# Optimization experiments

Hardware: AMD Instinct MI355X
Metric: run time of the kernel (lower is better)

The kernel has to match this reference:

```python
import jax, jax.numpy as jnp
import numpy as np

N = 262144
D = 512
H = 512
G = 1024


def setup_inputs() -> dict:
    key = jax.random.key(0)
    k1, k2, k3, k4 = jax.random.split(key, 4)
    embed = jax.random.normal(k1, (N, D), dtype=jnp.float32)
    batch_index = jnp.sort(jax.random.randint(k2, (N,), 0, G)).astype(jnp.int64)
    # nn.Linear weights: W_att [atten_hidden, embed_size], V_att [1, atten_hidden]
    W_att = jax.random.normal(k3, (H, D), dtype=jnp.float32) * (1.0 / np.sqrt(D))
    V_att = jax.random.normal(k4, (1, H), dtype=jnp.float32) * (1.0 / np.sqrt(H))
    return {"embed": embed, "batch_index": batch_index, "W_att": W_att, "V_att": V_att, "num_segments": G}


def reference(embed, batch_index, W_att, V_att, num_segments):
    # beta = V(tanh(W(embed))).squeeze(-1)  -> [N]
    beta = jnp.einsum('nh,oh->no', jnp.tanh(jnp.einsum('nd,hd->nh', embed, W_att)), V_att).squeeze(-1)
    # segment softmax (unnormalized exp, as in the original module)
    exp_beta = jnp.exp(beta)
    grouped_sum = jax.ops.segment_sum(exp_beta, batch_index, num_segments=num_segments)  # [G]
    alpha = exp_beta / grouped_sum[batch_index]  # [N]
    # scatter-weighted sum of node embeddings per graph -> [G, D]
    result = jax.ops.segment_sum(alpha[:, None] * embed, batch_index, num_segments=num_segments)
    return result
```

## Files before the change

### kernel.cpp

```cpp
#include <hip/hip_runtime.h>
#include <hip/hip_bf16.h>

#define D_DIM 512
#define H_DIM 512
#define G_SEG 1024
#define BM    64

typedef __attribute__((ext_vector_type(8))) short bf16x8;
typedef __attribute__((ext_vector_type(4))) float f32x4;
typedef unsigned int u32;
typedef unsigned short u16;

#define WS_S   0
#define WS_WB  8192

#define AS_BYTES  (BM * 1024)
#define BETA_OFF  AS_BYTES
#define EBS_OFF   (BETA_OFF + 4 * BM * 4)
#define SIDX_OFF  (EBS_OFF + BM * 4)
#define SCR_OFF   (SIDX_OFF + BM * 4)
#define LDS_TOTAL (SCR_OFF + 4 * 512 * 4)

static __device__ __forceinline__ u16 f2bf(float f) {
    __hip_bfloat16 h = __float2bfloat16(f);
    return *(u16*)&h;
}
static __device__ __forceinline__ float bf2f(u16 u) {
    return __uint_as_float(((u32)u) << 16);
}
static __device__ __forceinline__ float fast_tanh(float x) {
    float e = exp2f(x * 2.885390081777927f);
    return 1.0f - 2.0f * __builtin_amdgcn_rcpf(e + 1.0f);
}
static __device__ __forceinline__ void pack8(const float4& a, const float4& b, void* dst) {
    u16 h[8];
    h[0]=f2bf(a.x); h[1]=f2bf(a.y); h[2]=f2bf(a.z); h[3]=f2bf(a.w);
    h[4]=f2bf(b.x); h[5]=f2bf(b.y); h[6]=f2bf(b.z); h[7]=f2bf(b.w);
    *(uint4*)dst = *(uint4*)h;
}

__global__ __launch_bounds__(256)
void cvt_w(const float* __restrict__ W, u16* __restrict__ Wb) {
    int t   = blockIdx.x * 256 + threadIdx.x;
    int lhi = t & 3;
    int c   = (t >> 2) & 511;
    int k32 = t >> 11;
    const float* src = W + (size_t)c * 512 + k32 * 32 + lhi * 8;
    float4 f0 = *(const float4*)(src);
    float4 f1 = *(const float4*)(src + 4);
    pack8(f0, f1, Wb + (size_t)t * 8);
}

__global__ __launch_bounds__(256, 2)
void fused(const float* __restrict__ E, const int* __restrict__ BI,
           const u16* __restrict__ Wb, const float* __restrict__ V,
           float* __restrict__ out, float* __restrict__ S)
{
    extern __shared__ char smem[];
    const int tid = threadIdx.x;
    const int nodeBase = blockIdx.x * BM;
    const int l   = tid & 63;
    const int w   = tid >> 6;
    const int l15 = l & 15;
    const int lhi = l >> 4;

    const float* Eb = E + (size_t)nodeBase * 512;

#pragma unroll 1
    for (int p = 0; p < 4; ++p) {
        float4 L[8];
        const int ci0 = p * 1024 + tid * 4;
#pragma unroll
        for (int j = 0; j < 4; ++j) {
            int ci = ci0 + j;
            int row = ci >> 6, cc = ci & 63;
            const float* src = Eb + (size_t)row * 512 + cc * 8;
            L[2*j]   = *(const float4*)src;
            L[2*j+1] = *(const float4*)(src + 4);
        }
#pragma unroll
        for (int j = 0; j < 4; ++j) {
            int ci = ci0 + j;
            int row = ci >> 6, cc = ci & 63;
            int byte0 = row * 1024 + ((cc * 16) ^ ((row & 7) << 4));
            pack8(L[2*j], L[2*j+1], smem + byte0);
        }
    }
    __syncthreads();

    f32x4 acc[4][8];
#pragma unroll
    for (int m = 0; m < 4; ++m)
#pragma unroll
        for (int n = 0; n < 8; ++n) acc[m][n] = (f32x4){0.f, 0.f, 0.f, 0.f};

    const int bOffBase = ((w * 128 + l15) * 4 + lhi) * 16;
    const char* Wbb = (const char*)Wb;

    bf16x8 bA[8], bB[8];
#pragma unroll
    for (int n = 0; n < 8; ++n)
        bA[n] = *(const bf16x8*)(Wbb + bOffBase + n * 1024);

#pragma unroll 1
    for (int kk2 = 0; kk2 < 8; ++kk2) {
        {
            const char* Wn = Wbb + ((size_t)(2 * kk2 + 1) << 15);
#pragma unroll
            for (int n = 0; n < 8; ++n)
                bB[n] = *(const bf16x8*)(Wn + bOffBase + n * 1024);
            bf16x8 a[4];
            const int kbyte = (2 * kk2) * 64 + lhi * 16;
#pragma unroll
            for (int m = 0; m < 4; ++m) {
                int row = m * 16 + l15;
                a[m] = *(const bf16x8*)(smem + row * 1024 + (kbyte ^ ((row & 7) << 4)));
            }
#pragma unroll
            for (int m = 0; m < 4; ++m)
#pragma unroll
                for (int n = 0; n < 8; ++n)
                    acc[m][n] = __builtin_amdgcn_mfma_f32_16x16x32_bf16(a[m], bA[n], acc[m][n], 0, 0, 0);
        }
        {
            if (kk2 < 7) {
                const char* Wn = Wbb + ((size_t)(2 * kk2 + 2) << 15);
#pragma unroll
                for (int n = 0; n < 8; ++n)
                    bA[n] = *(const bf16x8*)(Wn + bOffBase + n * 1024);
            }
            bf16x8 a[4];
            const int kbyte = (2 * kk2 + 1) * 64 + lhi * 16;
#pragma unroll
            for (int m = 0; m < 4; ++m) {
                int row = m * 16 + l15;
                a[m] = *(const bf16x8*)(smem + row * 1024 + (kbyte ^ ((row & 7) << 4)));
            }
#pragma unroll
            for (int m = 0; m < 4; ++m)
#pragma unroll
                for (int n = 0; n < 8; ++n)
                    acc[m][n] = __builtin_amdgcn_mfma_f32_16x16x32_bf16(a[m], bB[n], acc[m][n], 0, 0, 0);
        }
    }

    float Vv[8];
#pragma unroll
    for (int n = 0; n < 8; ++n)
        Vv[n] = V[w * 128 + n * 16 + l15];

    float bsum[4][4];
#pragma unroll
    for (int m = 0; m < 4; ++m)
#pragma unroll
        for (int r = 0; r < 4; ++r) {
            float s = 0.f;
#pragma unroll
            for (int n = 0; n < 8; ++n)
                s += Vv[n] * fast_tanh(acc[m][n][r]);
            bsum[m][r] = s;
        }
#pragma unroll
    for (int off = 1; off <= 8; off <<= 1)
#pragma unroll
        for (int m = 0; m < 4; ++m)
#pragma unroll
            for (int r = 0; r < 4; ++r)
                bsum[m][r] += __shfl_xor(bsum[m][r], off, 64);

    float* betaP = (float*)(smem + BETA_OFF);
    if (l15 == 0) {
#pragma unroll
        for (int m = 0; m < 4; ++m)
#pragma unroll
            for (int r = 0; r < 4; ++r)
                betaP[w * BM + m * 16 + lhi * 4 + r] = bsum[m][r];
    }
    __syncthreads();

    float* ebs  = (float*)(smem + EBS_OFF);
    int*   sidx = (int*)(smem + SIDX_OFF);
    if (tid < BM) {
        float beta = betaP[tid] + betaP[BM + tid] + betaP[2 * BM + tid] + betaP[3 * BM + tid];
        float eb = expf(beta);
        ebs[tid] = eb;
        int g = BI[nodeBase + tid];
        sidx[tid] = g;
        int g0 = __shfl(g, 0, 64);
        if (__all(g == g0)) {
            float s = eb;
#pragma unroll
            for (int off = 1; off <= 32; off <<= 1)
                s += __shfl_xor(s, off, 64);
            if (l == 0) atomicAdd(&S[g], s);
        } else {
            atomicAdd(&S[g], eb);
        }
    }
    __syncthreads();

    {
        float* scr = (float*)(smem + SCR_OFF) + w * 512;
        const int rbase = w * 16;
        float a8[8];
#pragma unroll
        for (int j = 0; j < 8; ++j) a8[j] = 0.f;
        int gcur = sidx[rbase];

#pragma unroll 1
        for (int rr = 0; rr < 16; ++rr) {
            int r = rbase + rr;
            int g = sidx[r];
            if (g != gcur) {
                *(float4*)(scr + l * 8)     = make_float4(a8[0], a8[1], a8[2], a8[3]);
                *(float4*)(scr + l * 8 + 4) = make_float4(a8[4], a8[5], a8[6], a8[7]);
                asm volatile("s_waitcnt lgkmcnt(0)" ::: "memory");
#pragma unroll
                for (int j = 0; j < 8; ++j)
                    atomicAdd(&out[(size_t)gcur * 512 + j * 64 + l], scr[j * 64 + l]);
#pragma unroll
                for (int j = 0; j < 8; ++j) a8[j] = 0.f;
                gcur = g;
            }
            float wgt = ebs[r];
            bf16x8 v = *(const bf16x8*)(smem + r * 1024 + ((l * 16) ^ ((r & 7) << 4)));
#pragma unroll
            for (int j = 0; j < 8; ++j)
                a8[j] += wgt * bf2f((u16)v[j]);
        }
        *(float4*)(scr + l * 8)     = make_float4(a8[0], a8[1], a8[2], a8[3]);
        *(float4*)(scr + l * 8 + 4) = make_float4(a8[4], a8[5], a8[6], a8[7]);
        asm volatile("s_waitcnt lgkmcnt(0)" ::: "memory");
#pragma unroll
        for (int j = 0; j < 8; ++j)
            atomicAdd(&out[(size_t)gcur * 512 + j * 64 + l], scr[j * 64 + l]);
    }
}

__global__ __launch_bounds__(256)
void finalize_kernel(float* __restrict__ out, const float* __restrict__ S) {
    int idx = blockIdx.x * 256 + threadIdx.x;
    float s = S[idx >> 9];
    float v = out[idx];
    out[idx] = (s != 0.f) ? v * __builtin_amdgcn_rcpf(s) : 0.f;
}

extern "C" void kernel_launch(void* const* d_in, const int* in_sizes, int n_in,
                              void* d_out, int out_size, void* d_ws, size_t ws_size,
                              hipStream_t stream) {
    const float* E  = (const float*)d_in[0];
    const int*   BI = (const int*)d_in[1];
    const float* W  = (const float*)d_in[2];
    const float* V  = (const float*)d_in[3];
    float* out = (float*)d_out;
    char*  ws  = (char*)d_ws;
    const int Ntot = in_sizes[0] / D_DIM;

    float* S  = (float*)(ws + WS_S);
    u16*   Wb = (u16*)(ws + WS_WB);

    hipMemsetAsync(S, 0, G_SEG * 4, stream);
    hipMemsetAsync(out, 0, (size_t)out_size * 4, stream);
    hipFuncSetAttribute((const void*)fused,
                        hipFuncAttributeMaxDynamicSharedMemorySize, LDS_TOTAL);

    cvt_w<<<128, 256, 0, stream>>>(W, Wb);
    fused<<<Ntot / BM, 256, LDS_TOTAL, stream>>>(E, BI, Wb, V, out, S);
    finalize_kernel<<<out_size / 256, 256, 0, stream>>>(out, S);
}
```

Before: 356.3 us.

## Split fused kernel into GEMM-beta pass and separate fp32 weighted-sum pass

```diff
diff --git a/kernel.cpp b/kernel.cpp
--- a/kernel.cpp
+++ b/kernel.cpp
@@ -11,22 +11,17 @@
 typedef unsigned int u32;
 typedef unsigned short u16;
 
-#define WS_S   0
-#define WS_WB  8192
+#define WS_S    0
+#define WS_BETA 8192
+#define WS_WB   (8192 + (1u << 20))
 
 #define AS_BYTES  (BM * 1024)
 #define BETA_OFF  AS_BYTES
-#define EBS_OFF   (BETA_OFF + 4 * BM * 4)
-#define SIDX_OFF  (EBS_OFF + BM * 4)
-#define SCR_OFF   (SIDX_OFF + BM * 4)
-#define LDS_TOTAL (SCR_OFF + 4 * 512 * 4)
+#define LDS_K1    (BETA_OFF + 4 * BM * 4)
 
 static __device__ __forceinline__ u16 f2bf(float f) {
     __hip_bfloat16 h = __float2bfloat16(f);
     return *(u16*)&h;
-}
-static __device__ __forceinline__ float bf2f(u16 u) {
-    return __uint_as_float(((u32)u) << 16);
 }
 static __device__ __forceinline__ float fast_tanh(float x) {
     float e = exp2f(x * 2.885390081777927f);
@@ -52,9 +47,8 @@
 }
 
 __global__ __launch_bounds__(256, 2)
-void fused(const float* __restrict__ E, const int* __restrict__ BI,
-           const u16* __restrict__ Wb, const float* __restrict__ V,
-           float* __restrict__ out, float* __restrict__ S)
+void gemm_beta(const float* __restrict__ E, const u16* __restrict__ Wb,
+               const float* __restrict__ V, float* __restrict__ betaOut)
 {
     extern __shared__ char smem[];
     const int tid = threadIdx.x;
@@ -178,63 +172,58 @@
     }
     __syncthreads();
 
-    float* ebs  = (float*)(smem + EBS_OFF);
-    int*   sidx = (int*)(smem + SIDX_OFF);
     if (tid < BM) {
         float beta = betaP[tid] + betaP[BM + tid] + betaP[2 * BM + tid] + betaP[3 * BM + tid];
-        float eb = expf(beta);
-        ebs[tid] = eb;
-        int g = BI[nodeBase + tid];
-        sidx[tid] = g;
+        betaOut[nodeBase + tid] = beta;
+    }
+}
+
+__global__ __launch_bounds__(256)
+void wsum_eb(const float* __restrict__ E, const int* __restrict__ BI,
+             const float* __restrict__ beta, float* __restrict__ S,
+             float* __restrict__ out)
+{
+    __shared__ float al[256];
+    __shared__ int   sg[256];
+    const int t = threadIdx.x;
+    const int base = blockIdx.x * 256;
+    {
+        int n = base + t;
+        float eb = expf(beta[n]);
+        al[t] = eb;
+        int g = BI[n];
+        sg[t] = g;
         int g0 = __shfl(g, 0, 64);
         if (__all(g == g0)) {
             float s = eb;
 #pragma unroll
             for (int off = 1; off <= 32; off <<= 1)
                 s += __shfl_xor(s, off, 64);
-            if (l == 0) atomicAdd(&S[g], s);
+            if ((t & 63) == 0) atomicAdd(&S[g], s);
         } else {
             atomicAdd(&S[g], eb);
         }
     }
     __syncthreads();
 
-    {
-        float* scr = (float*)(smem + SCR_OFF) + w * 512;
-        const int rbase = w * 16;
-        float a8[8];
-#pragma unroll
-        for (int j = 0; j < 8; ++j) a8[j] = 0.f;
-        int gcur = sidx[rbase];
-
+    const int c4 = (t & 127) * 4;
+    const int rg = t >> 7;
+    float a0 = 0.f, a1 = 0.f, a2 = 0.f, a3 = 0.f;
+    int gcur = sg[rg];
 #pragma unroll 1
-        for (int rr = 0; rr < 16; ++rr) {
-            int r = rbase + rr;
-            int g = sidx[r];
-            if (g != gcur) {
-                *(float4*)(scr + l * 8)     = make_float4(a8[0], a8[1], a8[2], a8[3]);
-                *(float4*)(scr + l * 8 + 4) = make_float4(a8[4], a8[5], a8[6], a8[7]);
-                asm volatile("s_waitcnt lgkmcnt(0)" ::: "memory");
-#pragma unroll
-                for (int j = 0; j < 8; ++j)
-                    atomicAdd(&out[(size_t)gcur * 512 + j * 64 + l], scr[j * 64 + l]);
-#pragma unroll
-                for (int j = 0; j < 8; ++j) a8[j] = 0.f;
-                gcur = g;
-            }
-            float wgt = ebs[r];
-            bf16x8 v = *(const bf16x8*)(smem + r * 1024 + ((l * 16) ^ ((r & 7) << 4)));
-#pragma unroll
-            for (int j = 0; j < 8; ++j)
-                a8[j] += wgt * bf2f((u16)v[j]);
-        }
-        *(float4*)(scr + l * 8)     = make_float4(a8[0], a8[1], a8[2], a8[3]);
-        *(float4*)(scr + l * 8 + 4) = make_float4(a8[4], a8[5], a8[6], a8[7]);
-        asm volatile("s_waitcnt lgkmcnt(0)" ::: "memory");
-#pragma unroll
-        for (int j = 0; j < 8; ++j)
-            atomicAdd(&out[(size_t)gcur * 512 + j * 64 + l], scr[j * 64 + l]);
-    }
+    for (int r = rg; r < 256; r += 2) {
+        int g = sg[r];
+        if (g != gcur) {
+            float* o = out + (size_t)gcur * 512 + c4;
+            atomicAdd(o, a0); atomicAdd(o + 1, a1); atomicAdd(o + 2, a2); atomicAdd(o + 3, a3);
+            a0 = a1 = a2 = a3 = 0.f; gcur = g;
+        }
+        float wgt = al[r];
+        float4 v = *(const float4*)(E + (size_t)(base + r) * 512 + c4);
+        a0 += wgt * v.x; a1 += wgt * v.y; a2 += wgt * v.z; a3 += wgt * v.w;
+    }
+    float* o = out + (size_t)gcur * 512 + c4;
+    atomicAdd(o, a0); atomicAdd(o + 1, a1); atomicAdd(o + 2, a2); atomicAdd(o + 3, a3);
 }
 
 __global__ __launch_bounds__(256)
@@ -256,15 +245,17 @@
     char*  ws  = (char*)d_ws;
     const int Ntot = in_sizes[0] / D_DIM;
 
-    float* S  = (float*)(ws + WS_S);
-    u16*   Wb = (u16*)(ws + WS_WB);
+    float* S    = (float*)(ws + WS_S);
+    float* beta = (float*)(ws + WS_BETA);
+    u16*   Wb   = (u16*)(ws + WS_WB);
 
     hipMemsetAsync(S, 0, G_SEG * 4, stream);
     hipMemsetAsync(out, 0, (size_t)out_size * 4, stream);
-    hipFuncSetAttribute((const void*)fused,
-                        hipFuncAttributeMaxDynamicSharedMemorySize, LDS_TOTAL);
+    hipFuncSetAttribute((const void*)gemm_beta,
+                        hipFuncAttributeMaxDynamicSharedMemorySize, LDS_K1);
 
     cvt_w<<<128, 256, 0, stream>>>(W, Wb);
-    fused<<<Ntot / BM, 256, LDS_TOTAL, stream>>>(E, BI, Wb, V, out, S);
+    gemm_beta<<<Ntot / BM, 256, LDS_K1, stream>>>(E, Wb, V, beta);
+    wsum_eb<<<Ntot / 256, 256, 0, stream>>>(E, BI, beta, S, out);
     finalize_kernel<<<out_size / 256, 256, 0, stream>>>(out, S);
 }
```

Result: slower. 371.4 us (+4.2%).
